# Performance work log

Measured on AMD Instinct MI355X. Metric: run time of the kernel, lower is better.

Reference implementation:

```python
import jax, jax.numpy as jnp
import numpy as np

jax.config.update("jax_enable_x64", True)  # exact int64 fixed-point requantization

QMIN, QMAX = 0, 255  # 8-bit asymmetric activations


def _mul_m0_shift(acc, M0, shift):
    """gemmlowp-style fixed-point rescale: round((acc*M0)>>31) >> shift (rounding)."""
    prod = acc.astype(jnp.int64) * M0.astype(jnp.int64)
    nudge = jnp.where(prod >= 0, jnp.int64(1 << 30), jnp.int64(1 - (1 << 30)))
    hi = (prod + nudge) >> 31  # rounding-doubling high mul
    sh = shift.astype(jnp.int64)
    return (hi + (jnp.int64(1) << (sh - 1))) >> sh  # rounding right shift


def _requant(acc, M0, shift, z_out):
    return jnp.clip(_mul_m0_shift(acc, M0, shift) + z_out, QMIN, QMAX).astype(jnp.int32)


def _qconv(q, w, z_in, M0, shift, z_out, pad):
    # int8-style conv: subtract input zero-point, integer accumulate (exact in fp32
    # since |acc| < 2^24 by construction), then fixed-point requantize.
    xf = (q - z_in).astype(jnp.float32)
    acc = jax.lax.conv_general_dilated(
        xf, w, (1, 1), [(pad, pad), (pad, pad)],
        dimension_numbers=("NCHW", "OIHW", "NCHW"))
    return _requant(jnp.round(acc).astype(jnp.int64), M0, shift, z_out)


def _qbn(q, z_in, w, b, M0, shift, z_out):
    # fused quantized BN: per-channel integer affine + fixed-point requantize
    acc = (q.astype(jnp.int64) - z_in) * w.astype(jnp.int64)[None, :, None, None] \
          + b.astype(jnp.int64)[None, :, None, None]
    return _requant(acc, M0, shift, z_out)


def setup_inputs() -> dict:
    key = jax.random.key(0)
    ks = jax.random.split(key, 10)
    B, Cin, H, W = 32, 256, 56, 56
    width, Cout = 64, 256
    x = jax.random.randint(ks[0], (B, Cin, H, W), 0, 256, dtype=jnp.int32)
    w1 = jax.random.randint(ks[1], (width, Cin, 1, 1), -63, 64).astype(jnp.float32)
    w2 = jax.random.randint(ks[2], (width, width, 3, 3), -63, 64).astype(jnp.float32)
    w3 = jax.random.randint(ks[3], (Cout, width, 1, 1), -63, 64).astype(jnp.float32)
    bn1_w = jax.random.randint(ks[4], (width,), 100, 160).astype(jnp.float32)
    bn1_b = jax.random.randint(ks[5], (width,), -1000, 1000).astype(jnp.float32)
    bn2_w = jax.random.randint(ks[6], (width,), 100, 160).astype(jnp.float32)
    bn2_b = jax.random.randint(ks[7], (width,), -1000, 1000).astype(jnp.float32)
    bn3_w = jax.random.randint(ks[8], (Cout,), 100, 160).astype(jnp.float32)
    bn3_b = jax.random.randint(ks[9], (Cout,), -1000, 1000).astype(jnp.float32)
    conv_zin = jnp.array([128, 128, 128], jnp.int32)
    conv_m0 = jnp.array([1518500250] * 3, jnp.int32)
    conv_shift = jnp.array([9, 9, 9], jnp.int32)
    conv_zout = jnp.array([128, 128, 128], jnp.int32)
    bn_m0 = jnp.array([1073741824] * 3, jnp.int32)
    bn_shift = jnp.array([6, 6, 6], jnp.int32)
    bn_zout = jnp.array([128, 128, 128], jnp.int32)
    add_z = jnp.array([128, 128], jnp.int32)
    add_m0 = jnp.array([1073741824] * 2, jnp.int32)
    add_shift = jnp.array([1, 1], jnp.int32)
    add_zout = jnp.array(128, jnp.int32)
    return dict(x=x, w1=w1, w2=w2, w3=w3,
                bn1_w=bn1_w, bn1_b=bn1_b, bn2_w=bn2_w, bn2_b=bn2_b,
                bn3_w=bn3_w, bn3_b=bn3_b,
                conv_zin=conv_zin, conv_m0=conv_m0, conv_shift=conv_shift,
                conv_zout=conv_zout, bn_m0=bn_m0, bn_shift=bn_shift,
                bn_zout=bn_zout, add_z=add_z, add_m0=add_m0,
                add_shift=add_shift, add_zout=add_zout)


def reference(x, w1, w2, w3, bn1_w, bn1_b, bn2_w, bn2_b, bn3_w, bn3_b,
              conv_zin, conv_m0, conv_shift, conv_zout,
              bn_m0, bn_shift, bn_zout,
              add_z, add_m0, add_shift, add_zout):
    identity = x  # a_bit == target_bit -> rescale_matrix path skipped, conv_x = x
    out = _qconv(x, w1, conv_zin[0], conv_m0[0], conv_shift[0], conv_zout[0], 0)
    out = _qbn(out, conv_zout[0], bn1_w, bn1_b, bn_m0[0], bn_shift[0], bn_zout[0])
    out = _qconv(out, w2, conv_zin[1], conv_m0[1], conv_shift[1], conv_zout[1], 1)
    out = _qbn(out, conv_zout[1], bn2_w, bn2_b, bn_m0[1], bn_shift[1], bn_zout[1])
    out = _qconv(out, w3, conv_zin[2], conv_m0[2], conv_shift[2], conv_zout[2], 0)
    out = _qbn(out, conv_zout[2], bn3_w, bn3_b, bn_m0[2], bn_shift[2], bn_zout[2])
    # QuantizedAdd: rescale both branches to the output scale, add, clamp
    ra = _mul_m0_shift(identity.astype(jnp.int64) - add_z[0], add_m0[0], add_shift[0])
    rb = _mul_m0_shift(out.astype(jnp.int64) - add_z[1], add_m0[1], add_shift[1])
    return jnp.clip(ra + rb + add_zout, QMIN, QMAX).astype(jnp.int32)
```

## Files before the change

### kernel.cpp

```cpp
#include <hip/hip_runtime.h>


typedef int v4i __attribute__((ext_vector_type(4)));

#define BATCH 32
#define CIN 256
#define CMID 64
#define HW 3136
#define W56 56

#define WP_BYTES ((size_t)68 * 64 * 16)
#define WSUM_BYTES ((size_t)64 * 4)

__device__ __forceinline__ int rq_apply(int acc, int m0, long long cp, long long cn,
                                        int shm1, int zo) {
    long long prod = (long long)acc * m0;
    prod += (prod >= 0) ? cp : cn;
    int hi = (int)((unsigned long long)prod >> 32);
    int v = (hi >> shm1) + zo;
    return v < 0 ? 0 : (v > 255 ? 255 : v);
}

__device__ __forceinline__ int ms_apply(int xin, int m0, long long cp, long long cn,
                                        int shm1) {
    long long prod = (long long)xin * m0;
    prod += (prod >= 0) ? cp : cn;
    return ((int)((unsigned long long)prod >> 32)) >> shm1;
}

__device__ __forceinline__ unsigned int pk4x(int a0, int a1, int a2, int a3) {
    unsigned p01 = __builtin_amdgcn_perm((unsigned)a1, (unsigned)a0, 0x00000400u);
    unsigned p23 = __builtin_amdgcn_perm((unsigned)a3, (unsigned)a2, 0x04000000u);
    return __builtin_amdgcn_perm(p23, p01, 0x07060100u);
}

__device__ __forceinline__ v4i pack16f(const float* src, int stride) {
    v4i r;
#pragma unroll
    for (int d = 0; d < 4; ++d) {
        unsigned int u = 0;
#pragma unroll
        for (int by = 0; by < 4; ++by) {
            int v = (int)src[(d * 4 + by) * stride];
            u |= ((unsigned int)(v & 255)) << (8 * by);
        }
        r[d] = (int)u;
    }
    return r;
}

__global__ __launch_bounds__(256) void k_prep(
    const float* __restrict__ w1, const float* __restrict__ w2,
    const float* __restrict__ w3, v4i* __restrict__ wp, int* __restrict__ wsum)
{
    if (blockIdx.x < 17) {
        int id = blockIdx.x * 256 + threadIdx.x;
        int fid = id >> 6, lane = id & 63;
        int col = lane & 15, ci0 = (lane >> 4) * 16;
        const float* src;
        int stride;
        if (fid < 16) {
            int wv = fid >> 2, ks = fid & 3;
            src = w1 + (size_t)(wv * 16 + col) * 256 + ks * 64 + ci0;
            stride = 1;
        } else if (fid < 52) {
            int i = fid - 16, wv = i / 9, t = i - wv * 9;
            src = w2 + ((size_t)(wv * 16 + col) * 64 + ci0) * 9 + t;
            stride = 9;
        } else {
            int s = fid - 52;
            src = w3 + (size_t)(s * 16 + col) * 64 + ci0;
            stride = 1;
        }
        wp[fid * 64 + lane] = pack16f(src, stride);
    } else {
        int ch = threadIdx.x >> 2, t4 = threadIdx.x & 3;
        int s = 0;
        for (int i = 0; i < 64; ++i) s += (int)w1[(size_t)ch * 256 + t4 * 64 + i];
        s += __shfl_xor(s, 1);
        s += __shfl_xor(s, 2);
        if (t4 == 0) wsum[ch] = s;
    }
}

__global__ __launch_bounds__(256, 5) void k_conv1(
    const int* __restrict__ x, const v4i* __restrict__ wp1,
    const int* __restrict__ wsum1,
    const float* __restrict__ bn_w, const float* __restrict__ bn_b,
    const int* __restrict__ conv_zin, const int* __restrict__ conv_m0,
    const int* __restrict__ conv_shift, const int* __restrict__ conv_zout,
    const int* __restrict__ bn_m0, const int* __restrict__ bn_shift,
    const int* __restrict__ bn_zout, signed char* __restrict__ t1)
{
    __shared__ v4i sm[320];
    const int tid = threadIdx.x, lane = tid & 63, wv = tid >> 6;
    const int col = lane & 15, koff = lane >> 4;
    const int b = blockIdx.y;
    const int hw0 = blockIdx.x * 64;
    const int co0 = wv * 16;

    v4i a[4];
#pragma unroll
    for (int ks = 0; ks < 4; ++ks) a[ks] = wp1[(wv * 4 + ks) * 64 + lane];

    const int cg = tid & 15, q = tid >> 4;
    const int* xbase = x + (size_t)b * CIN * HW + hw0 + 4 * q;

    v4i xa[4], xa2[4];
#pragma unroll
    for (int j = 0; j < 4; ++j)
        xa[j] = *(const v4i*)(xbase + (size_t)(cg * 4 + j) * HW);

    v4i acc[4];
#pragma unroll
    for (int i = 0; i < 4; ++i) acc[i] = (v4i){0, 0, 0, 0};

    unsigned* smx = (unsigned*)sm;
#pragma unroll
    for (int ks = 0; ks < 4; ++ks) {
        if (ks) __syncthreads();
#pragma unroll
        for (int p = 0; p < 4; ++p) {
            unsigned pkd = pk4x(xa[0][p], xa[1][p], xa[2][p], xa[3][p]) ^ 0x80808080u;
            smx[(q * 4 + p) * 20 + cg] = pkd;
        }
        __syncthreads();
        if (ks < 3) {
#pragma unroll
            for (int j = 0; j < 4; ++j)
                xa2[j] = *(const v4i*)(xbase + (size_t)((ks + 1) * 64 + cg * 4 + j) * HW);
        }
#pragma unroll
        for (int nt = 0; nt < 4; ++nt) {
            v4i bf = sm[(nt * 16 + col) * 5 + koff];
            acc[nt] = __builtin_amdgcn_mfma_i32_16x16x64_i8(a[ks], bf, acc[nt], 0, 0, 0);
        }
        if (ks < 3) {
#pragma unroll
            for (int j = 0; j < 4; ++j) xa[j] = xa2[j];
        }
    }

    const int zin = conv_zin[0];
    const int corr0 = 128 - zin;
    const int cm0 = conv_m0[0], csh = conv_shift[0], czo = conv_zout[0];
    const int bm0 = bn_m0[0], bsh = bn_shift[0], bzo = bn_zout[0];
    const int zin2 = conv_zin[1];
    const long long cbv = 1LL << (30 + csh);
    const long long ccp = cbv + (1LL << 30), ccn = cbv + 1 - (1LL << 30);
    const int cshm1 = csh - 1;
    const long long bbv = 1LL << (30 + bsh);
    const long long bcp = bbv + (1LL << 30), bcn = bbv + 1 - (1LL << 30);
    const int bshm1 = bsh - 1;
    const int rowb = koff * 4;
    int bw[4], bbx[4], ws[4];
#pragma unroll
    for (int r = 0; r < 4; ++r) {
        bw[r] = (int)bn_w[co0 + rowb + r];
        bbx[r] = (int)bn_b[co0 + rowb + r] - czo * bw[r];
        ws[r] = wsum1[co0 + rowb + r];
    }
#pragma unroll
    for (int nt = 0; nt < 4; ++nt) {
        int n = b * HW + hw0 + nt * 16 + col;
        int e[4];
#pragma unroll
        for (int r = 0; r < 4; ++r) {
            int av = acc[nt][r] + corr0 * ws[r];
            int qv = rq_apply(av, cm0, ccp, ccn, cshm1, czo);
            int a2 = qv * bw[r] + bbx[r];
            int q2 = rq_apply(a2, bm0, bcp, bcn, bshm1, bzo);
            e[r] = q2 - zin2;
        }
        *(unsigned*)(t1 + (size_t)n * 64 + co0 + rowb) = pk4x(e[0], e[1], e[2], e[3]);
    }
}

__global__ __launch_bounds__(256, 5) void k_conv23(
    const signed char* __restrict__ t1, const v4i* __restrict__ wp2,
    const v4i* __restrict__ wp3,
    const float* __restrict__ bn2_w, const float* __restrict__ bn2_b,
    const float* __restrict__ bn3_w, const float* __restrict__ bn3_b,
    const int* __restrict__ x,
    const int* __restrict__ conv_zin, const int* __restrict__ conv_m0,
    const int* __restrict__ conv_shift, const int* __restrict__ conv_zout,
    const int* __restrict__ bn_m0, const int* __restrict__ bn_shift,
    const int* __restrict__ bn_zout,
    const int* __restrict__ add_z, const int* __restrict__ add_m0,
    const int* __restrict__ add_shift, const int* __restrict__ add_zout,
    int* __restrict__ out)
{
    __shared__ v4i sm[840];
    __shared__ v4i t2s[320];
    const int tid = threadIdx.x, lane = tid & 63, wv = tid >> 6;
    const int col = lane & 15, koff = lane >> 4;
    const int b = blockIdx.y;
    const int r0 = blockIdx.x;
    const int co0 = wv * 16, rowb = koff * 4;

    v4i a[9];
#pragma unroll
    for (int t = 0; t < 9; ++t) a[t] = wp2[(wv * 9 + t) * 64 + lane];

    const v4i* t1v = (const v4i*)t1;
#pragma unroll
    for (int k = 0; k < 3; ++k) {
        int idx = tid + k * 256;
        if (idx < 672) {
            int pixl = idx >> 2, part = idx & 3;
            int lrow = pixl / W56, gw = pixl - lrow * W56;
            int grow = r0 - 1 + lrow;
            v4i v = (v4i){0, 0, 0, 0};
            if ((unsigned)grow < 56u)
                v = t1v[((size_t)b * HW + grow * W56 + gw) * 4 + part];
            sm[pixl * 5 + part] = v;
        }
    }
    __syncthreads();

    v4i acc[4];
#pragma unroll
    for (int i = 0; i < 4; ++i) acc[i] = (v4i){0, 0, 0, 0};

#pragma unroll
    for (int kh = 0; kh < 3; ++kh) {
#pragma unroll
        for (int kw = 0; kw < 3; ++kw) {
            v4i af = a[kh * 3 + kw];
#pragma unroll
            for (int nt = 0; nt < 4; ++nt) {
                int sw = nt * 16 + col + kw - 1;
                bool valid = (unsigned)sw < 56u;
                v4i bf = sm[(kh * W56 + (valid ? sw : 0)) * 5 + koff];
                if (!valid) { bf[0] = 0; bf[1] = 0; bf[2] = 0; bf[3] = 0; }
                acc[nt] = __builtin_amdgcn_mfma_i32_16x16x64_i8(af, bf, acc[nt], 0, 0, 0);
            }
        }
    }

    v4i a3x[4];
#pragma unroll
    for (int s = 0; s < 4; ++s) a3x[s] = wp3[(wv * 4 + s) * 64 + lane];

    int pxc[4];
#pragma unroll
    for (int nt = 0; nt < 4; ++nt) {
        int px = nt * 16 + col;
        pxc[nt] = px < 56 ? px : 55;
    }
    const size_t xoff = (size_t)b * CIN * HW + (size_t)rowb * HW + r0 * W56;
    const int* xb = x + xoff;
    int* ob = out + xoff;

    int xv[4][4];
#pragma unroll
    for (int nt = 0; nt < 4; ++nt)
#pragma unroll
        for (int r = 0; r < 4; ++r)
            xv[nt][r] = xb[(size_t)(wv * 64 + r) * HW + pxc[nt]];

    {
        const int cm0 = conv_m0[1], csh = conv_shift[1], czo = conv_zout[1];
        const int bm0 = bn_m0[1], bsh = bn_shift[1], bzo = bn_zout[1];
        const int zin3 = conv_zin[2];
        const long long cbv = 1LL << (30 + csh);
        const long long ccp = cbv + (1LL << 30), ccn = cbv + 1 - (1LL << 30);
        const int cshm1 = csh - 1;
        const long long bbv = 1LL << (30 + bsh);
        const long long bcp = bbv + (1LL << 30), bcn = bbv + 1 - (1LL << 30);
        const int bshm1 = bsh - 1;
        int bw[4], bbx[4];
#pragma unroll
        for (int r = 0; r < 4; ++r) {
            bw[r] = (int)bn2_w[co0 + rowb + r];
            bbx[r] = (int)bn2_b[co0 + rowb + r] - czo * bw[r];
        }
#pragma unroll
        for (int nt = 0; nt < 4; ++nt) {
            int pix = nt * 16 + col;
            int e[4];
#pragma unroll
            for (int r = 0; r < 4; ++r) {
                int qv = rq_apply(acc[nt][r], cm0, ccp, ccn, cshm1, czo);
                int a2 = qv * bw[r] + bbx[r];
                int q2 = rq_apply(a2, bm0, bcp, bcn, bshm1, bzo);
                e[r] = q2 - zin3;
            }
            *(unsigned*)((char*)t2s + (size_t)(pix * 5 + wv) * 16 + koff * 4) =
                pk4x(e[0], e[1], e[2], e[3]);
        }
    }
    __syncthreads();

    const int cm0 = conv_m0[2], csh = conv_shift[2], czo = conv_zout[2];
    const int bm0 = bn_m0[2], bsh = bn_shift[2], bzo = bn_zout[2];
    const long long cb3 = 1LL << (30 + csh);
    const long long ccp = cb3 + (1LL << 30), ccn = cb3 + 1 - (1LL << 30);
    const int cshm1 = csh - 1;
    const long long bb3 = 1LL << (30 + bsh);
    const long long bcp = bb3 + (1LL << 30), bcn = bb3 + 1 - (1LL << 30);
    const int bshm1 = bsh - 1;
    const int az0 = add_z[0], az1 = add_z[1];
    const int am0 = add_m0[0], am1 = add_m0[1];
    const int ash0 = add_shift[0], ash1 = add_shift[1];
    const long long a0b = 1LL << (30 + ash0);
    const long long acp0 = a0b + (1LL << 30), acn0 = a0b + 1 - (1LL << 30);
    const int ashm0 = ash0 - 1;
    const long long a1b = 1LL << (30 + ash1);
    const long long acp1 = a1b + (1LL << 30), acn1 = a1b + 1 - (1LL << 30);
    const int ashm1 = ash1 - 1;
    const int azout = add_zout[0];

#pragma unroll
    for (int s = 0; s < 4; ++s) {
        const int c0 = wv * 64 + s * 16;
        int xn[4][4];
        if (s < 3) {
#pragma unroll
            for (int nt = 0; nt < 4; ++nt)
#pragma unroll
                for (int r = 0; r < 4; ++r)
                    xn[nt][r] = xb[(size_t)(c0 + 16 + r) * HW + pxc[nt]];
        }
        v4i acc3[4];
#pragma unroll
        for (int i = 0; i < 4; ++i) acc3[i] = (v4i){0, 0, 0, 0};
#pragma unroll
        for (int nt = 0; nt < 4; ++nt) {
            v4i bf = t2s[(nt * 16 + col) * 5 + koff];
            acc3[nt] = __builtin_amdgcn_mfma_i32_16x16x64_i8(a3x[s], bf, acc3[nt], 0, 0, 0);
        }
        int bw3[4], bbx3[4];
#pragma unroll
        for (int r = 0; r < 4; ++r) {
            bw3[r] = (int)bn3_w[c0 + rowb + r];
            bbx3[r] = (int)bn3_b[c0 + rowb + r] - czo * bw3[r];
        }
#pragma unroll
        for (int nt = 0; nt < 4; ++nt) {
            bool st = (nt * 16 + col) < 56;
#pragma unroll
            for (int r = 0; r < 4; ++r) {
                int qv = rq_apply(acc3[nt][r], cm0, ccp, ccn, cshm1, czo);
                int a2 = qv * bw3[r] + bbx3[r];
                int q2 = rq_apply(a2, bm0, bcp, bcn, bshm1, bzo);
                int ra = ms_apply(xv[nt][r] - az0, am0, acp0, acn0, ashm0);
                int rb = ms_apply(q2 - az1, am1, acp1, acn1, ashm1);
                int res = ra + rb + azout;
                res = res < 0 ? 0 : (res > 255 ? 255 : res);
                if (st) ob[(size_t)(c0 + r) * HW + pxc[nt]] = res;
            }
        }
        if (s < 3) {
#pragma unroll
            for (int nt = 0; nt < 4; ++nt)
#pragma unroll
                for (int r = 0; r < 4; ++r)
                    xv[nt][r] = xn[nt][r];
        }
    }
}

extern "C" void kernel_launch(void* const* d_in, const int* in_sizes, int n_in,
                              void* d_out, int out_size, void* d_ws, size_t ws_size,
                              hipStream_t stream) {
    const int* x = (const int*)d_in[0];
    const float* w1 = (const float*)d_in[1];
    const float* w2 = (const float*)d_in[2];
    const float* w3 = (const float*)d_in[3];
    const float* bn1_w = (const float*)d_in[4];
    const float* bn1_b = (const float*)d_in[5];
    const float* bn2_w = (const float*)d_in[6];
    const float* bn2_b = (const float*)d_in[7];
    const float* bn3_w = (const float*)d_in[8];
    const float* bn3_b = (const float*)d_in[9];
    const int* conv_zin = (const int*)d_in[10];
    const int* conv_m0 = (const int*)d_in[11];
    const int* conv_shift = (const int*)d_in[12];
    const int* conv_zout = (const int*)d_in[13];
    const int* bn_m0 = (const int*)d_in[14];
    const int* bn_shift = (const int*)d_in[15];
    const int* bn_zout = (const int*)d_in[16];
    const int* add_z = (const int*)d_in[17];
    const int* add_m0 = (const int*)d_in[18];
    const int* add_shift = (const int*)d_in[19];
    const int* add_zout = (const int*)d_in[20];

    v4i* wp = (v4i*)d_ws;
    int* wsum1 = (int*)((char*)d_ws + WP_BYTES);
    signed char* t1 = (signed char*)d_ws + WP_BYTES + WSUM_BYTES;

    const v4i* wp1 = wp;
    const v4i* wp2 = wp + 16 * 64;
    const v4i* wp3 = wp + 52 * 64;

    k_prep<<<dim3(18), dim3(256), 0, stream>>>(w1, w2, w3, wp, wsum1);
    k_conv1<<<dim3(49, 32), dim3(256), 0, stream>>>(x, wp1, wsum1, bn1_w, bn1_b,
        conv_zin, conv_m0, conv_shift, conv_zout, bn_m0, bn_shift, bn_zout, t1);
    k_conv23<<<dim3(56, 32), dim3(256), 0, stream>>>(t1, wp2, wp3,
        bn2_w, bn2_b, bn3_w, bn3_b, x,
        conv_zin, conv_m0, conv_shift, conv_zout, bn_m0, bn_shift, bn_zout,
        add_z, add_m0, add_shift, add_zout, (int*)d_out);
}
```

Baseline: 307.0 us.

## Widen conv1 pixel tiles and stage residual input via async LDS loads in conv23

k_conv1 now handles 112 pixels per block instead of 64: each thread loads 8 channels with 64-bit LDS stores, using 7 MFMA tiles over 28 blocks per image. This amortises weight loads and cuts the block count. k_conv23 replaces register-held residual x reads with double-buffered global_load_lds staging into a 32KB shared buffer, overlapped with the conv2 compute, and hoists the BN3 and weight loads. It uses manual waitcnt and sched barriers, and the larger LDS use lowers occupancy.

```diff
diff --git a/kernel.cpp b/kernel.cpp
--- a/kernel.cpp
+++ b/kernel.cpp
@@ -32,6 +32,12 @@
     unsigned p01 = __builtin_amdgcn_perm((unsigned)a1, (unsigned)a0, 0x00000400u);
     unsigned p23 = __builtin_amdgcn_perm((unsigned)a3, (unsigned)a2, 0x04000000u);
     return __builtin_amdgcn_perm(p23, p01, 0x07060100u);
+}
+
+__device__ __forceinline__ void gll16(const int* g, void* l) {
+    __builtin_amdgcn_global_load_lds(
+        (const __attribute__((address_space(1))) unsigned int*)g,
+        (__attribute__((address_space(3))) unsigned int*)l, 16, 0, 0);
 }
 
 __device__ __forceinline__ v4i pack16f(const float* src, int stride) {
@@ -83,7 +89,7 @@
     }
 }
 
-__global__ __launch_bounds__(256, 5) void k_conv1(
+__global__ __launch_bounds__(256, 4) void k_conv1(
     const int* __restrict__ x, const v4i* __restrict__ wp1,
     const int* __restrict__ wsum1,
     const float* __restrict__ bn_w, const float* __restrict__ bn_b,
@@ -92,52 +98,58 @@
     const int* __restrict__ bn_m0, const int* __restrict__ bn_shift,
     const int* __restrict__ bn_zout, signed char* __restrict__ t1)
 {
-    __shared__ v4i sm[320];
+    __shared__ v4i sm[560];
     const int tid = threadIdx.x, lane = tid & 63, wv = tid >> 6;
     const int col = lane & 15, koff = lane >> 4;
     const int b = blockIdx.y;
-    const int hw0 = blockIdx.x * 64;
+    const int hw0 = blockIdx.x * 112;
     const int co0 = wv * 16;
 
     v4i a[4];
 #pragma unroll
     for (int ks = 0; ks < 4; ++ks) a[ks] = wp1[(wv * 4 + ks) * 64 + lane];
 
-    const int cg = tid & 15, q = tid >> 4;
+    const int cg = tid & 7, q = tid >> 3;
+    const bool act = q < 28;
     const int* xbase = x + (size_t)b * CIN * HW + hw0 + 4 * q;
 
-    v4i xa[4], xa2[4];
-#pragma unroll
-    for (int j = 0; j < 4; ++j)
-        xa[j] = *(const v4i*)(xbase + (size_t)(cg * 4 + j) * HW);
-
-    v4i acc[4];
-#pragma unroll
-    for (int i = 0; i < 4; ++i) acc[i] = (v4i){0, 0, 0, 0};
-
-    unsigned* smx = (unsigned*)sm;
+    v4i xa[8], xa2[8];
+    if (act) {
+#pragma unroll
+        for (int j = 0; j < 8; ++j)
+            xa[j] = *(const v4i*)(xbase + (size_t)(cg * 8 + j) * HW);
+    }
+
+    v4i acc[7];
+#pragma unroll
+    for (int i = 0; i < 7; ++i) acc[i] = (v4i){0, 0, 0, 0};
+
+    unsigned long long* smu = (unsigned long long*)sm;
 #pragma unroll
     for (int ks = 0; ks < 4; ++ks) {
         if (ks) __syncthreads();
-#pragma unroll
-        for (int p = 0; p < 4; ++p) {
-            unsigned pkd = pk4x(xa[0][p], xa[1][p], xa[2][p], xa[3][p]) ^ 0x80808080u;
-            smx[(q * 4 + p) * 20 + cg] = pkd;
+        if (act) {
+#pragma unroll
+            for (int p = 0; p < 4; ++p) {
+                unsigned lo = pk4x(xa[0][p], xa[1][p], xa[2][p], xa[3][p]) ^ 0x80808080u;
+                unsigned hi = pk4x(xa[4][p], xa[5][p], xa[6][p], xa[7][p]) ^ 0x80808080u;
+                smu[(q * 4 + p) * 10 + cg] = ((unsigned long long)hi << 32) | lo;
+            }
         }
         __syncthreads();
-        if (ks < 3) {
-#pragma unroll
-            for (int j = 0; j < 4; ++j)
-                xa2[j] = *(const v4i*)(xbase + (size_t)((ks + 1) * 64 + cg * 4 + j) * HW);
-        }
-#pragma unroll
-        for (int nt = 0; nt < 4; ++nt) {
+        if (ks < 3 && act) {
+#pragma unroll
+            for (int j = 0; j < 8; ++j)
+                xa2[j] = *(const v4i*)(xbase + (size_t)((ks + 1) * 64 + cg * 8 + j) * HW);
+        }
+#pragma unroll
+        for (int nt = 0; nt < 7; ++nt) {
             v4i bf = sm[(nt * 16 + col) * 5 + koff];
             acc[nt] = __builtin_amdgcn_mfma_i32_16x16x64_i8(a[ks], bf, acc[nt], 0, 0, 0);
         }
         if (ks < 3) {
 #pragma unroll
-            for (int j = 0; j < 4; ++j) xa[j] = xa2[j];
+            for (int j = 0; j < 8; ++j) xa[j] = xa2[j];
         }
     }
 
@@ -161,7 +173,7 @@
         ws[r] = wsum1[co0 + rowb + r];
     }
 #pragma unroll
-    for (int nt = 0; nt < 4; ++nt) {
+    for (int nt = 0; nt < 7; ++nt) {
         int n = b * HW + hw0 + nt * 16 + col;
         int e[4];
 #pragma unroll
@@ -176,7 +188,7 @@
     }
 }
 
-__global__ __launch_bounds__(256, 5) void k_conv23(
+__global__ __launch_bounds__(256, 3) void k_conv23(
     const signed char* __restrict__ t1, const v4i* __restrict__ wp2,
     const v4i* __restrict__ wp3,
     const float* __restrict__ bn2_w, const float* __restrict__ bn2_b,
@@ -192,6 +204,7 @@
 {
     __shared__ v4i sm[840];
     __shared__ v4i t2s[320];
+    __shared__ int xs[2][64][64];
     const int tid = threadIdx.x, lane = tid & 63, wv = tid >> 6;
     const int col = lane & 15, koff = lane >> 4;
     const int b = blockIdx.y;
@@ -201,6 +214,9 @@
     v4i a[9];
 #pragma unroll
     for (int t = 0; t < 9; ++t) a[t] = wp2[(wv * 9 + t) * 64 + lane];
+    v4i a3x[4];
+#pragma unroll
+    for (int s = 0; s < 4; ++s) a3x[s] = wp3[(wv * 4 + s) * 64 + lane];
 
     const v4i* t1v = (const v4i*)t1;
 #pragma unroll
@@ -218,6 +234,20 @@
     }
     __syncthreads();
 
+    const int* gsrc = x + (size_t)b * CIN * HW + (size_t)r0 * W56;
+    int pxl = (lane & 15) * 4;
+    if (pxl > 52) pxl = 52;
+    const int chsub = lane >> 4;
+    auto stage = [&](int t) {
+        const int chb = wv * 64 + t * 16 + chsub;
+#pragma unroll
+        for (int j = 0; j < 4; ++j)
+            gll16(gsrc + (size_t)(chb + j * 4) * HW + pxl,
+                  &xs[t & 1][wv * 16 + j * 4][0]);
+    };
+    stage(0);
+    stage(1);
+
     v4i acc[4];
 #pragma unroll
     for (int i = 0; i < 4; ++i) acc[i] = (v4i){0, 0, 0, 0};
@@ -237,27 +267,6 @@
             }
         }
     }
-
-    v4i a3x[4];
-#pragma unroll
-    for (int s = 0; s < 4; ++s) a3x[s] = wp3[(wv * 4 + s) * 64 + lane];
-
-    int pxc[4];
-#pragma unroll
-    for (int nt = 0; nt < 4; ++nt) {
-        int px = nt * 16 + col;
-        pxc[nt] = px < 56 ? px : 55;
-    }
-    const size_t xoff = (size_t)b * CIN * HW + (size_t)rowb * HW + r0 * W56;
-    const int* xb = x + xoff;
-    int* ob = out + xoff;
-
-    int xv[4][4];
-#pragma unroll
-    for (int nt = 0; nt < 4; ++nt)
-#pragma unroll
-        for (int r = 0; r < 4; ++r)
-            xv[nt][r] = xb[(size_t)(wv * 64 + r) * HW + pxc[nt]];
 
     {
         const int cm0 = conv_m0[1], csh = conv_shift[1], czo = conv_zout[1];
@@ -290,7 +299,6 @@
                 pk4x(e[0], e[1], e[2], e[3]);
         }
     }
-    __syncthreads();
 
     const int cm0 = conv_m0[2], csh = conv_shift[2], czo = conv_zout[2];
     const int bm0 = bn_m0[2], bsh = bn_shift[2], bzo = bn_zout[2];
@@ -310,53 +318,53 @@
     const long long acp1 = a1b + (1LL << 30), acn1 = a1b + 1 - (1LL << 30);
     const int ashm1 = ash1 - 1;
     const int azout = add_zout[0];
-
-#pragma unroll
-    for (int s = 0; s < 4; ++s) {
-        const int c0 = wv * 64 + s * 16;
-        int xn[4][4];
-        if (s < 3) {
-#pragma unroll
-            for (int nt = 0; nt < 4; ++nt)
-#pragma unroll
-                for (int r = 0; r < 4; ++r)
-                    xn[nt][r] = xb[(size_t)(c0 + 16 + r) * HW + pxc[nt]];
-        }
+    int bw3[4][4], bbx3[4][4];
+#pragma unroll
+    for (int s = 0; s < 4; ++s)
+#pragma unroll
+        for (int r = 0; r < 4; ++r) {
+            bw3[s][r] = (int)bn3_w[wv * 64 + s * 16 + rowb + r];
+            bbx3[s][r] = (int)bn3_b[wv * 64 + s * 16 + rowb + r] - czo * bw3[s][r];
+        }
+
+    __syncthreads();
+
+    int* ob = out + (size_t)b * CIN * HW + (size_t)r0 * W56;
+
+#pragma unroll
+    for (int t = 0; t < 4; ++t) {
+        const int c0 = wv * 64 + t * 16;
         v4i acc3[4];
 #pragma unroll
         for (int i = 0; i < 4; ++i) acc3[i] = (v4i){0, 0, 0, 0};
 #pragma unroll
         for (int nt = 0; nt < 4; ++nt) {
             v4i bf = t2s[(nt * 16 + col) * 5 + koff];
-            acc3[nt] = __builtin_amdgcn_mfma_i32_16x16x64_i8(a3x[s], bf, acc3[nt], 0, 0, 0);
-        }
-        int bw3[4], bbx3[4];
-#pragma unroll
-        for (int r = 0; r < 4; ++r) {
-            bw3[r] = (int)bn3_w[c0 + rowb + r];
-            bbx3[r] = (int)bn3_b[c0 + rowb + r] - czo * bw3[r];
-        }
+            acc3[nt] = __builtin_amdgcn_mfma_i32_16x16x64_i8(a3x[t], bf, acc3[nt], 0, 0, 0);
+        }
+        asm volatile("s_waitcnt vmcnt(4)" ::: "memory");
+        __builtin_amdgcn_sched_barrier(0);
 #pragma unroll
         for (int nt = 0; nt < 4; ++nt) {
-            bool st = (nt * 16 + col) < 56;
+            int px = nt * 16 + col;
+            bool st = px < 56;
 #pragma unroll
             for (int r = 0; r < 4; ++r) {
+                int xr = xs[t & 1][co0 + rowb + r][px];
                 int qv = rq_apply(acc3[nt][r], cm0, ccp, ccn, cshm1, czo);
-                int a2 = qv * bw3[r] + bbx3[r];
+                int a2 = qv * bw3[t][r] + bbx3[t][r];
                 int q2 = rq_apply(a2, bm0, bcp, bcn, bshm1, bzo);
-                int ra = ms_apply(xv[nt][r] - az0, am0, acp0, acn0, ashm0);
+                int ra = ms_apply(xr - az0, am0, acp0, acn0, ashm0);
                 int rb = ms_apply(q2 - az1, am1, acp1, acn1, ashm1);
                 int res = ra + rb + azout;
                 res = res < 0 ? 0 : (res > 255 ? 255 : res);
-                if (st) ob[(size_t)(c0 + r) * HW + pxc[nt]] = res;
+                if (st) ob[(size_t)(c0 + rowb + r) * HW + px] = res;
             }
         }
-        if (s < 3) {
-#pragma unroll
-            for (int nt = 0; nt < 4; ++nt)
-#pragma unroll
-                for (int r = 0; r < 4; ++r)
-                    xv[nt][r] = xn[nt][r];
+        if (t < 2) {
+            asm volatile("s_waitcnt lgkmcnt(0)" ::: "memory");
+            __builtin_amdgcn_sched_barrier(0);
+            stage(t + 2);
         }
     }
 }
@@ -395,7 +403,7 @@
     const v4i* wp3 = wp + 52 * 64;
 
     k_prep<<<dim3(18), dim3(256), 0, stream>>>(w1, w2, w3, wp, wsum1);
-    k_conv1<<<dim3(49, 32), dim3(256), 0, stream>>>(x, wp1, wsum1, bn1_w, bn1_b,
+    k_conv1<<<dim3(28, 32), dim3(256), 0, stream>>>(x, wp1, wsum1, bn1_w, bn1_b,
         conv_zin, conv_m0, conv_shift, conv_zout, bn_m0, bn_shift, bn_zout, t1);
     k_conv23<<<dim3(56, 32), dim3(256), 0, stream>>>(t1, wp2, wp3,
         bn2_w, bn2_b, bn3_w, bn3_b, x,
```

Measured after the change: 287.6 us. 6.3% less time.
